# Kernel tuning notes

Measured on AMD Instinct MI355X. Metric: run time of the kernel, lower is better.

Reference implementation:

```python
import jax, jax.numpy as jnp
import numpy as np

TOP_K = 2
EPS = 1e-6

def setup_inputs() -> dict:
    key = jax.random.key(0)
    ks = jax.random.split(key, 6)
    Bt, S, D, E, R = 4, 4096, 1024, 8, 4
    s = lambda d: 1.0 / np.sqrt(d)
    return {
        "x": jax.random.normal(ks[0], (Bt, S, D), jnp.float32),
        "W_base": jax.random.normal(ks[1], (D, D), jnp.float32) * s(D),
        "b_base": jax.random.normal(ks[2], (D,), jnp.float32) * 0.02,
        "W_router": jax.random.normal(ks[3], (E, D), jnp.float32) * s(D),
        "A": jax.random.normal(ks[4], (E, D, R), jnp.float32) * s(D),
        "B": jax.random.normal(ks[5], (E, R, D), jnp.float32) * s(R),
    }

def reference(x, W_base, b_base, W_router, A, B):
    # frozen base linear: [b,s,d] @ [out,d]^T + bias
    base_out = jnp.einsum('bsd,od->bso', x, W_base) + b_base
    # router softmax gate over experts
    logits = jnp.einsum('bsd,ed->bse', x, W_router)
    gate = jax.nn.softmax(logits, axis=-1)
    # top-k scatter-mask (values kept are the gate values themselves)
    topv, topi = jax.lax.top_k(gate, TOP_K)                    # [b,s,k]
    mask = jnp.sum(jax.nn.one_hot(topi, gate.shape[-1], dtype=gate.dtype), axis=-2)
    gate = gate * mask
    gate = gate / (jnp.sum(gate, axis=-1, keepdims=True) + EPS)
    # batched rank-4 LoRA experts, gating applied in low-rank space
    h = jnp.einsum('bsd,edr->bser', x, A)                      # [b,s,E,r]
    hg = h * gate[..., None]                                   # weight before up-proj
    lora_out = jnp.einsum('bser,ero->bso', hg, B)
    return base_out + lora_out
```

## Files before the change

### kernel.cpp

```cpp
#include <hip/hip_runtime.h>
#include <cstdint>

typedef __attribute__((ext_vector_type(8))) short short8;
typedef __attribute__((ext_vector_type(4))) float f32x4;

__device__ inline unsigned short f2bf(float f){
  union { float f; uint32_t u; } v; v.f = f;
  uint32_t r = v.u + 0x7FFFu + ((v.u >> 16) & 1u);
  return (unsigned short)(r >> 16);
}

#define GLL(gp, lp) __builtin_amdgcn_global_load_lds(              \
    (const __attribute__((address_space(1))) void*)(gp),           \
    (__attribute__((address_space(3))) void*)(lp), 16, 0, 0)

__global__ __launch_bounds__(256) void kconv(const float* __restrict__ W,
                                             const float* __restrict__ A,
                                             const float* __restrict__ Bm,
                                             unsigned short* __restrict__ Wb,
                                             unsigned short* __restrict__ BTt,
                                             unsigned short* __restrict__ W2b){
  int i = blockIdx.x * 256 + threadIdx.x;
  Wb[i] = f2bf(W[i]);
  if (i < 32768){
    int o = i >> 5, c = i & 31;
    BTt[i] = f2bf(Bm[(size_t)c*1024 + o]);
    int n = i >> 10, d = i & 1023;
    W2b[i] = f2bf(A[(((size_t)(n>>2))*1024 + d)*4 + (n&3)]);
  }
}

__global__ __launch_bounds__(256) void kxl(const float* __restrict__ x,
                                           const float* __restrict__ Wr,
                                           unsigned short* __restrict__ xb,
                                           float* __restrict__ gate){
  __shared__ float wr[8192];
  const int tid  = threadIdx.x;
  const int lane = tid & 63;
  const int w    = tid >> 6;
  {
    const float4* s  = (const float4*)Wr;
    float4*       d4 = (float4*)wr;
    #pragma unroll
    for (int j=0;j<8;j++) d4[j*256+tid] = s[j*256+tid];
  }
  __syncthreads();
  const float4* wr4 = (const float4*)wr;
  #pragma unroll 1
  for (int tt=0; tt<4; tt++){
    const size_t tok = (size_t)blockIdx.x*16 + w*4 + tt;
    const float4* xr = (const float4*)(x + tok*1024);
    ushort4*      xd = (ushort4*)(xb + tok*1024);
    float4 xv[4];
    #pragma unroll
    for (int c=0;c<4;c++){
      xv[c] = xr[c*64 + lane];
      ushort4 o4; o4.x=f2bf(xv[c].x); o4.y=f2bf(xv[c].y);
      o4.z=f2bf(xv[c].z); o4.w=f2bf(xv[c].w);
      xd[c*64 + lane] = o4;
    }
    float p[8];
    #pragma unroll
    for (int e=0;e<8;e++){
      float a = 0.f;
      #pragma unroll
      for (int c=0;c<4;c++){
        float4 wv = wr4[e*256 + c*64 + lane];
        a += xv[c].x*wv.x + xv[c].y*wv.y + xv[c].z*wv.z + xv[c].w*wv.w;
      }
      p[e] = a;
    }
    #pragma unroll
    for (int off=32; off; off>>=1){
      #pragma unroll
      for (int e=0;e<8;e++) p[e] += __shfl_xor(p[e], off, 64);
    }
    if (lane == 0){
      float mx = p[0];
      #pragma unroll
      for (int e=1;e<8;e++) mx = fmaxf(mx, p[e]);
      float ex[8], s2 = 0.f;
      #pragma unroll
      for (int e=0;e<8;e++){ ex[e] = __expf(p[e]-mx); s2 += ex[e]; }
      int i1 = 0; float v1 = ex[0];
      #pragma unroll
      for (int e=1;e<8;e++) if (ex[e] > v1){ v1 = ex[e]; i1 = e; }
      int i2 = -1; float v2 = -1.f;
      #pragma unroll
      for (int e=0;e<8;e++) if (e != i1 && ex[e] > v2){ v2 = ex[e]; i2 = e; }
      float g1 = v1/s2, g2 = v2/s2;
      float rs = 1.f/(g1 + g2 + 1e-6f);
      float* go = gate + tok*8;
      #pragma unroll
      for (int e=0;e<8;e++) go[e] = (e==i1 ? g1 : (e==i2 ? g2 : 0.f)) * rs;
    }
  }
}

__global__ __launch_bounds__(256) void kh(const unsigned short* __restrict__ xbp,
                                          const unsigned short* __restrict__ W2b,
                                          const float* __restrict__ gate,
                                          unsigned short* __restrict__ HG){
  const int tid  = threadIdx.x;
  const int lane = tid & 63;
  const int wid  = tid >> 6;
  const int lrow = lane & 15;
  const int lk   = (lane >> 4) * 8;
  const int tok0 = blockIdx.x*64 + wid*16;
  f32x4 acc0 = {0.f,0.f,0.f,0.f}, acc1 = {0.f,0.f,0.f,0.f};
  const unsigned short* b0 = W2b + (size_t)lrow*1024 + lk;
  const unsigned short* b1 = W2b + (size_t)(16+lrow)*1024 + lk;
  const unsigned short* ar = xbp + (size_t)(tok0+lrow)*1024 + lk;
  #pragma unroll 4
  for (int ks=0; ks<32; ks++){
    short8 av  = *(const short8*)(ar + ks*32);
    short8 bv0 = *(const short8*)(b0 + ks*32);
    short8 bv1 = *(const short8*)(b1 + ks*32);
    acc0 = __builtin_amdgcn_mfma_f32_16x16x32_bf16(av, bv0, acc0, 0, 0, 0);
    acc1 = __builtin_amdgcn_mfma_f32_16x16x32_bf16(av, bv1, acc1, 0, 0, 0);
  }
  #pragma unroll
  for (int j=0;j<4;j++){
    int tok = tok0 + (lane>>4)*4 + j;
    float g0 = gate[(size_t)tok*8 + (lrow>>2)];
    float g1 = gate[(size_t)tok*8 + 4 + (lrow>>2)];
    HG[(size_t)tok*32 + lrow]      = f2bf(acc0[j]*g0);
    HG[(size_t)tok*32 + 16 + lrow] = f2bf(acc1[j]*g1);
  }
}

__global__ __launch_bounds__(512, 2) void kgemm2(const unsigned short* __restrict__ xb,
                                                 const unsigned short* __restrict__ Wb,
                                                 const unsigned short* __restrict__ BTt,
                                                 const unsigned short* __restrict__ HG,
                                                 const float* __restrict__ bias,
                                                 float* __restrict__ out){
  __shared__ char lds[65536];
  const int tid  = threadIdx.x;
  const int lane = tid & 63;
  const int w    = tid >> 6;
  const int xcd  = blockIdx.x & 7, jj = blockIdx.x >> 3;
  const int nblk = xcd >> 1;
  const int mblk = (xcd & 1) * 32 + jj;
  const int m0 = mblk << 8, n0 = nblk << 8;
  const int wm = w >> 2, wn = w & 3;
  const int lrow = lane & 15;
  const int lkb  = (lane >> 4) << 4;

  int offA[8], offB[4];
  #pragma unroll
  for (int fm=0; fm<8; fm++){ int r = wm*128 + fm*16 + lrow; offA[fm] = r*64 + (lkb ^ (((r>>1)&3)<<4)); }
  #pragma unroll
  for (int fn=0; fn<4; fn++){ int r = wn*64  + fn*16 + lrow; offB[fn] = r*64 + (lkb ^ (((r>>1)&3)<<4)); }

  const int Rb0 = (w&3)*16 + (w>>2)*128 + (lane>>2);
  const int Rb1 = Rb0 + 64;
  const int ob  = (lane&3)*16;
  const int sw0 = ((Rb0>>1)&3)<<4, sw1 = ((Rb1>>1)&3)<<4;
  const char* Ag0 = (const char*)xb + (size_t)(m0+Rb0)*2048 + (ob ^ sw0);
  const char* Ag1 = (const char*)xb + (size_t)(m0+Rb1)*2048 + (ob ^ sw1);
  const char* Bg0 = (const char*)Wb + (size_t)(n0+Rb0)*2048 + (ob ^ sw0);
  const char* Bg1 = (const char*)Wb + (size_t)(n0+Rb1)*2048 + (ob ^ sw1);
  const int dH0 = ((w&3)*16 + (w>>2)*128)*64 + lane*16;
  const int dH1 = dH0 + 4096;

  f32x4 acc[8][4];
  #pragma unroll
  for (int a=0;a<8;a++)
    #pragma unroll
    for (int b=0;b<4;b++) acc[a][b] = (f32x4){0.f,0.f,0.f,0.f};

  GLL(Ag0 +  0, lds + dH0);            GLL(Ag1 +  0, lds + dH1);
  GLL(Bg0 +  0, lds + 32768 + dH0);    GLL(Bg1 +  0, lds + 32768 + dH1);
  GLL(Ag0 + 64, lds + 16384 + dH0);    GLL(Bg0 + 64, lds + 49152 + dH0);

  #pragma unroll 1
  for (int t = 0; t < 32; ++t){
    const int s = t & 1;
    const char* Ab = lds + s*16384;
    const char* Bb = lds + 32768 + s*16384;
    if (t < 31){
      const int s1 = (t+1)&1;
      GLL(Ag1 + (t+1)*64, lds + s1*16384 + dH1);
      GLL(Bg1 + (t+1)*64, lds + 32768 + s1*16384 + dH1);
      asm volatile("s_waitcnt vmcnt(4)" ::: "memory");
    } else {
      asm volatile("s_waitcnt vmcnt(0)" ::: "memory");
    }
    __builtin_amdgcn_s_barrier();
    short8 bf[4];
    #pragma unroll
    for (int fn=0;fn<4;fn++) bf[fn] = *(const short8*)(Bb + offB[fn]);
    short8 af[4];
    #pragma unroll
    for (int fm=0;fm<4;fm++) af[fm] = *(const short8*)(Ab + offA[fm]);
    __builtin_amdgcn_s_setprio(1);
    #pragma unroll
    for (int fm=0;fm<4;fm++)
      #pragma unroll
      for (int fn=0;fn<4;fn++)
        acc[fm][fn] = __builtin_amdgcn_mfma_f32_16x16x32_bf16(af[fm], bf[fn], acc[fm][fn], 0, 0, 0);
    __builtin_amdgcn_s_setprio(0);
    __builtin_amdgcn_s_barrier();
    if (t < 30){
      const int s2 = t & 1;
      GLL(Ag0 + (t+2)*64, lds + s2*16384 + dH0);
      GLL(Bg0 + (t+2)*64, lds + 32768 + s2*16384 + dH0);
    }
    short8 ag[4];
    #pragma unroll
    for (int fm=0;fm<4;fm++) ag[fm] = *(const short8*)(Ab + offA[4+fm]);
    __builtin_amdgcn_s_setprio(1);
    #pragma unroll
    for (int fm=0;fm<4;fm++)
      #pragma unroll
      for (int fn=0;fn<4;fn++)
        acc[4+fm][fn] = __builtin_amdgcn_mfma_f32_16x16x32_bf16(ag[fm], bf[fn], acc[4+fm][fn], 0, 0, 0);
    __builtin_amdgcn_s_setprio(0);
    __builtin_amdgcn_s_barrier();
  }

  {
    const char* Hg0 = (const char*)HG  + (size_t)(m0+Rb0)*64 + (ob ^ sw0);
    const char* Hg1 = (const char*)HG  + (size_t)(m0+Rb1)*64 + (ob ^ sw1);
    const char* Tg0 = (const char*)BTt + (size_t)(n0+Rb0)*64 + (ob ^ sw0);
    const char* Tg1 = (const char*)BTt + (size_t)(n0+Rb1)*64 + (ob ^ sw1);
    GLL(Hg0, lds + dH0);          GLL(Hg1, lds + dH1);
    GLL(Tg0, lds + 32768 + dH0);  GLL(Tg1, lds + 32768 + dH1);
    asm volatile("s_waitcnt vmcnt(0)" ::: "memory");
    __builtin_amdgcn_s_barrier();
    short8 hb[4];
    #pragma unroll
    for (int fn=0;fn<4;fn++) hb[fn] = *(const short8*)(lds + 32768 + offB[fn]);
    #pragma unroll
    for (int fm=0;fm<8;fm++){
      short8 ha = *(const short8*)(lds + offA[fm]);
      #pragma unroll
      for (int fn=0;fn<4;fn++)
        acc[fm][fn] = __builtin_amdgcn_mfma_f32_16x16x32_bf16(ha, hb[fn], acc[fm][fn], 0, 0, 0);
    }
  }

  #pragma unroll
  for (int fn=0;fn<4;fn++){
    int col = n0 + wn*64 + fn*16 + lrow;
    float bv = bias[col];
    #pragma unroll
    for (int fm=0;fm<8;fm++){
      int rb = m0 + wm*128 + fm*16 + (lane>>4)*4;
      #pragma unroll
      for (int j=0;j<4;j++)
        out[(size_t)(rb+j)*1024 + col] = acc[fm][fn][j] + bv;
    }
  }
}

extern "C" void kernel_launch(void* const* d_in, const int* in_sizes, int n_in,
                              void* d_out, int out_size, void* d_ws, size_t ws_size,
                              hipStream_t stream){
  const float* x  = (const float*)d_in[0];
  const float* W  = (const float*)d_in[1];
  const float* bb = (const float*)d_in[2];
  const float* Wr = (const float*)d_in[3];
  const float* A  = (const float*)d_in[4];
  const float* Bm = (const float*)d_in[5];
  float* out = (float*)d_out;
  char* ws = (char*)d_ws;

  unsigned short* Wb   = (unsigned short*)(ws + 0);
  unsigned short* BTt  = (unsigned short*)(ws + 2097152);
  unsigned short* W2b  = (unsigned short*)(ws + 2162688);
  float*          gate = (float*)         (ws + 2228224);
  unsigned short* HG   = (unsigned short*)(ws + 2752512);
  unsigned short* xb   = (unsigned short*)(ws + 3801088);

  kconv<<<4096, 256, 0, stream>>>(W, A, Bm, Wb, BTt, W2b);
  kxl<<<1024, 256, 0, stream>>>(x, Wr, xb, gate);
  kh<<<256, 256, 0, stream>>>(xb, W2b, gate, HG);
  kgemm2<<<256, 512, 0, stream>>>(xb, Wb, BTt, HG, bb, out);
}
```

Before: 97.46 us.

## Rework router kernel and switch main GEMM to smaller 128x128 tiles

The router/convert kernel now assigns 8 lanes per token and 32 tokens per block, halving the block count and shortening the shuffle reduction. The main GEMM drops from 256x256 tiles with 512 threads and a double-buffered, hand-pipelined load schedule to 128x128 tiles with 256 threads, a single-buffered 64-wide K stage, an XOR swizzle and plain __syncthreads. The low-rank LoRA term is now loaded straight from global memory rather than staged through LDS. This trades the overlap of loads with MFMA and the reuse of larger tiles for more blocks and higher occupancy (4 blocks per CU), and it fetches more total global traffic.

```diff
diff --git a/kernel.cpp b/kernel.cpp
--- a/kernel.cpp
+++ b/kernel.cpp
@@ -30,14 +30,14 @@
   }
 }
 
-__global__ __launch_bounds__(256) void kxl(const float* __restrict__ x,
-                                           const float* __restrict__ Wr,
-                                           unsigned short* __restrict__ xb,
-                                           float* __restrict__ gate){
+__global__ __launch_bounds__(256) void kxl2(const float* __restrict__ x,
+                                            const float* __restrict__ Wr,
+                                            unsigned short* __restrict__ xb,
+                                            float* __restrict__ gate){
   __shared__ float wr[8192];
   const int tid  = threadIdx.x;
   const int lane = tid & 63;
-  const int w    = tid >> 6;
+  const int wid  = tid >> 6;
   {
     const float4* s  = (const float4*)Wr;
     float4*       d4 = (float4*)wr;
@@ -45,55 +45,46 @@
     for (int j=0;j<8;j++) d4[j*256+tid] = s[j*256+tid];
   }
   __syncthreads();
-  const float4* wr4 = (const float4*)wr;
-  #pragma unroll 1
-  for (int tt=0; tt<4; tt++){
-    const size_t tok = (size_t)blockIdx.x*16 + w*4 + tt;
-    const float4* xr = (const float4*)(x + tok*1024);
-    ushort4*      xd = (ushort4*)(xb + tok*1024);
-    float4 xv[4];
-    #pragma unroll
-    for (int c=0;c<4;c++){
-      xv[c] = xr[c*64 + lane];
-      ushort4 o4; o4.x=f2bf(xv[c].x); o4.y=f2bf(xv[c].y);
-      o4.z=f2bf(xv[c].z); o4.w=f2bf(xv[c].w);
-      xd[c*64 + lane] = o4;
-    }
-    float p[8];
+  const int tk  = lane >> 3, ln8 = lane & 7;
+  const size_t tok = (size_t)blockIdx.x*32 + wid*8 + tk;
+  const float4* xr = (const float4*)(x + tok*1024);
+  ushort4*      xd = (ushort4*)(xb + tok*1024);
+  const float4* wv = (const float4*)wr;
+  float p[8] = {0.f,0.f,0.f,0.f,0.f,0.f,0.f,0.f};
+  #pragma unroll 4
+  for (int it=0; it<32; it++){
+    float4 v = xr[it*8 + ln8];
+    ushort4 o; o.x=f2bf(v.x); o.y=f2bf(v.y); o.z=f2bf(v.z); o.w=f2bf(v.w);
+    xd[it*8 + ln8] = o;
     #pragma unroll
     for (int e=0;e<8;e++){
-      float a = 0.f;
-      #pragma unroll
-      for (int c=0;c<4;c++){
-        float4 wv = wr4[e*256 + c*64 + lane];
-        a += xv[c].x*wv.x + xv[c].y*wv.y + xv[c].z*wv.z + xv[c].w*wv.w;
-      }
-      p[e] = a;
-    }
-    #pragma unroll
-    for (int off=32; off; off>>=1){
-      #pragma unroll
-      for (int e=0;e<8;e++) p[e] += __shfl_xor(p[e], off, 64);
-    }
-    if (lane == 0){
-      float mx = p[0];
-      #pragma unroll
-      for (int e=1;e<8;e++) mx = fmaxf(mx, p[e]);
-      float ex[8], s2 = 0.f;
-      #pragma unroll
-      for (int e=0;e<8;e++){ ex[e] = __expf(p[e]-mx); s2 += ex[e]; }
-      int i1 = 0; float v1 = ex[0];
-      #pragma unroll
-      for (int e=1;e<8;e++) if (ex[e] > v1){ v1 = ex[e]; i1 = e; }
-      int i2 = -1; float v2 = -1.f;
-      #pragma unroll
-      for (int e=0;e<8;e++) if (e != i1 && ex[e] > v2){ v2 = ex[e]; i2 = e; }
-      float g1 = v1/s2, g2 = v2/s2;
-      float rs = 1.f/(g1 + g2 + 1e-6f);
-      float* go = gate + tok*8;
-      #pragma unroll
-      for (int e=0;e<8;e++) go[e] = (e==i1 ? g1 : (e==i2 ? g2 : 0.f)) * rs;
-    }
+      float4 wq = wv[e*256 + it*8 + ln8];
+      p[e] += v.x*wq.x + v.y*wq.y + v.z*wq.z + v.w*wq.w;
+    }
+  }
+  #pragma unroll
+  for (int off=1; off<8; off<<=1){
+    #pragma unroll
+    for (int e=0;e<8;e++) p[e] += __shfl_xor(p[e], off, 64);
+  }
+  if (ln8 == 0){
+    float mx = p[0];
+    #pragma unroll
+    for (int e=1;e<8;e++) mx = fmaxf(mx, p[e]);
+    float ex[8], s2 = 0.f;
+    #pragma unroll
+    for (int e=0;e<8;e++){ ex[e] = __expf(p[e]-mx); s2 += ex[e]; }
+    int i1 = 0; float v1 = ex[0];
+    #pragma unroll
+    for (int e=1;e<8;e++) if (ex[e] > v1){ v1 = ex[e]; i1 = e; }
+    int i2 = -1; float v2 = -1.f;
+    #pragma unroll
+    for (int e=0;e<8;e++) if (e != i1 && ex[e] > v2){ v2 = ex[e]; i2 = e; }
+    float g1 = v1/s2, g2 = v2/s2;
+    float rs = 1.f/(g1 + g2 + 1e-6f);
+    float* go = gate + tok*8;
+    #pragma unroll
+    for (int e=0;e<8;e++) go[e] = (e==i1 ? g1 : (e==i2 ? g2 : 0.f)) * rs;
   }
 }
 
@@ -129,116 +120,85 @@
   }
 }
 
-__global__ __launch_bounds__(512, 2) void kgemm2(const unsigned short* __restrict__ xb,
+__global__ __launch_bounds__(256, 4) void kgemm7(const unsigned short* __restrict__ xb,
                                                  const unsigned short* __restrict__ Wb,
                                                  const unsigned short* __restrict__ BTt,
                                                  const unsigned short* __restrict__ HG,
                                                  const float* __restrict__ bias,
                                                  float* __restrict__ out){
-  __shared__ char lds[65536];
+  __shared__ __attribute__((aligned(128))) char lds[32768];
   const int tid  = threadIdx.x;
   const int lane = tid & 63;
   const int w    = tid >> 6;
-  const int xcd  = blockIdx.x & 7, jj = blockIdx.x >> 3;
-  const int nblk = xcd >> 1;
-  const int mblk = (xcd & 1) * 32 + jj;
-  const int m0 = mblk << 8, n0 = nblk << 8;
-  const int wm = w >> 2, wn = w & 3;
+  const int mblk = blockIdx.x & 127;
+  const int nblk = blockIdx.x >> 7;
+  const int m0 = mblk << 7, n0 = nblk << 7;
+  const int wm = w >> 1, wn = w & 1;
   const int lrow = lane & 15;
-  const int lkb  = (lane >> 4) << 4;
-
-  int offA[8], offB[4];
-  #pragma unroll
-  for (int fm=0; fm<8; fm++){ int r = wm*128 + fm*16 + lrow; offA[fm] = r*64 + (lkb ^ (((r>>1)&3)<<4)); }
-  #pragma unroll
-  for (int fn=0; fn<4; fn++){ int r = wn*64  + fn*16 + lrow; offB[fn] = r*64 + (lkb ^ (((r>>1)&3)<<4)); }
-
-  const int Rb0 = (w&3)*16 + (w>>2)*128 + (lane>>2);
-  const int Rb1 = Rb0 + 64;
-  const int ob  = (lane&3)*16;
-  const int sw0 = ((Rb0>>1)&3)<<4, sw1 = ((Rb1>>1)&3)<<4;
-  const char* Ag0 = (const char*)xb + (size_t)(m0+Rb0)*2048 + (ob ^ sw0);
-  const char* Ag1 = (const char*)xb + (size_t)(m0+Rb1)*2048 + (ob ^ sw1);
-  const char* Bg0 = (const char*)Wb + (size_t)(n0+Rb0)*2048 + (ob ^ sw0);
-  const char* Bg1 = (const char*)Wb + (size_t)(n0+Rb1)*2048 + (ob ^ sw1);
-  const int dH0 = ((w&3)*16 + (w>>2)*128)*64 + lane*16;
-  const int dH1 = dH0 + 4096;
-
-  f32x4 acc[8][4];
-  #pragma unroll
-  for (int a=0;a<8;a++)
-    #pragma unroll
-    for (int b=0;b<4;b++) acc[a][b] = (f32x4){0.f,0.f,0.f,0.f};
-
-  GLL(Ag0 +  0, lds + dH0);            GLL(Ag1 +  0, lds + dH1);
-  GLL(Bg0 +  0, lds + 32768 + dH0);    GLL(Bg1 +  0, lds + 32768 + dH1);
-  GLL(Ag0 + 64, lds + 16384 + dH0);    GLL(Bg0 + 64, lds + 49152 + dH0);
+  const int q    = lane >> 4;
+
+  const int rowL = lane >> 3;
+  const int colb = ((lane & 7) ^ rowL) << 4;
+  const int rb   = w * 32;
+  const char* Ag = (const char*)xb + ((size_t)(m0 + rb + rowL) << 11) + colb;
+  const char* Bg = (const char*)Wb + ((size_t)(n0 + rb + rowL) << 11) + colb;
+  char* Ad = lds +         rb*128 + lane*16;
+  char* Bd = lds + 16384 + rb*128 + lane*16;
+
+  int offA[4][2], offB[4][2];
+  #pragma unroll
+  for (int f=0; f<4; f++){
+    int ra = wm*64 + f*16 + lrow;
+    int rbn = wn*64 + f*16 + lrow;
+    #pragma unroll
+    for (int kk=0; kk<2; kk++){
+      offA[f][kk] =         ra*128  + ((((kk*4+q) ^ (ra  & 7)) << 4));
+      offB[f][kk] = 16384 + rbn*128 + ((((kk*4+q) ^ (rbn & 7)) << 4));
+    }
+  }
+
+  f32x4 acc[4][4];
+  #pragma unroll
+  for (int a2=0;a2<4;a2++)
+    #pragma unroll
+    for (int b2=0;b2<4;b2++) acc[a2][b2] = (f32x4){0.f,0.f,0.f,0.f};
 
   #pragma unroll 1
-  for (int t = 0; t < 32; ++t){
-    const int s = t & 1;
-    const char* Ab = lds + s*16384;
-    const char* Bb = lds + 32768 + s*16384;
-    if (t < 31){
-      const int s1 = (t+1)&1;
-      GLL(Ag1 + (t+1)*64, lds + s1*16384 + dH1);
-      GLL(Bg1 + (t+1)*64, lds + 32768 + s1*16384 + dH1);
-      asm volatile("s_waitcnt vmcnt(4)" ::: "memory");
-    } else {
-      asm volatile("s_waitcnt vmcnt(0)" ::: "memory");
-    }
-    __builtin_amdgcn_s_barrier();
-    short8 bf[4];
-    #pragma unroll
-    for (int fn=0;fn<4;fn++) bf[fn] = *(const short8*)(Bb + offB[fn]);
-    short8 af[4];
-    #pragma unroll
-    for (int fm=0;fm<4;fm++) af[fm] = *(const short8*)(Ab + offA[fm]);
-    __builtin_amdgcn_s_setprio(1);
+  for (int t = 0; t < 16; ++t){
+    __syncthreads();
+    #pragma unroll
+    for (int i=0;i<4;i++) GLL(Ag + (size_t)i*16384 + t*128, Ad + i*1024);
+    #pragma unroll
+    for (int i=0;i<4;i++) GLL(Bg + (size_t)i*16384 + t*128, Bd + i*1024);
+    __syncthreads();
+    #pragma unroll
+    for (int kk=0; kk<2; kk++){
+      short8 a[4], b[4];
+      #pragma unroll
+      for (int f=0; f<4; f++){
+        a[f] = *(const short8*)(lds + offA[f][kk]);
+        b[f] = *(const short8*)(lds + offB[f][kk]);
+      }
+      #pragma unroll
+      for (int fm=0;fm<4;fm++)
+        #pragma unroll
+        for (int fn=0;fn<4;fn++)
+          acc[fm][fn] = __builtin_amdgcn_mfma_f32_16x16x32_bf16(a[fm], b[fn], acc[fm][fn], 0, 0, 0);
+    }
+  }
+
+  {
+    short8 ha[4], hb[4];
+    #pragma unroll
+    for (int f=0; f<4; f++){
+      ha[f] = *(const short8*)(HG  + (size_t)(m0 + wm*64 + f*16 + lrow)*32 + q*8);
+      hb[f] = *(const short8*)(BTt + (size_t)(n0 + wn*64 + f*16 + lrow)*32 + q*8);
+    }
     #pragma unroll
     for (int fm=0;fm<4;fm++)
       #pragma unroll
       for (int fn=0;fn<4;fn++)
-        acc[fm][fn] = __builtin_amdgcn_mfma_f32_16x16x32_bf16(af[fm], bf[fn], acc[fm][fn], 0, 0, 0);
-    __builtin_amdgcn_s_setprio(0);
-    __builtin_amdgcn_s_barrier();
-    if (t < 30){
-      const int s2 = t & 1;
-      GLL(Ag0 + (t+2)*64, lds + s2*16384 + dH0);
-      GLL(Bg0 + (t+2)*64, lds + 32768 + s2*16384 + dH0);
-    }
-    short8 ag[4];
-    #pragma unroll
-    for (int fm=0;fm<4;fm++) ag[fm] = *(const short8*)(Ab + offA[4+fm]);
-    __builtin_amdgcn_s_setprio(1);
-    #pragma unroll
-    for (int fm=0;fm<4;fm++)
-      #pragma unroll
-      for (int fn=0;fn<4;fn++)
-        acc[4+fm][fn] = __builtin_amdgcn_mfma_f32_16x16x32_bf16(ag[fm], bf[fn], acc[4+fm][fn], 0, 0, 0);
-    __builtin_amdgcn_s_setprio(0);
-    __builtin_amdgcn_s_barrier();
-  }
-
-  {
-    const char* Hg0 = (const char*)HG  + (size_t)(m0+Rb0)*64 + (ob ^ sw0);
-    const char* Hg1 = (const char*)HG  + (size_t)(m0+Rb1)*64 + (ob ^ sw1);
-    const char* Tg0 = (const char*)BTt + (size_t)(n0+Rb0)*64 + (ob ^ sw0);
-    const char* Tg1 = (const char*)BTt + (size_t)(n0+Rb1)*64 + (ob ^ sw1);
-    GLL(Hg0, lds + dH0);          GLL(Hg1, lds + dH1);
-    GLL(Tg0, lds + 32768 + dH0);  GLL(Tg1, lds + 32768 + dH1);
-    asm volatile("s_waitcnt vmcnt(0)" ::: "memory");
-    __builtin_amdgcn_s_barrier();
-    short8 hb[4];
-    #pragma unroll
-    for (int fn=0;fn<4;fn++) hb[fn] = *(const short8*)(lds + 32768 + offB[fn]);
-    #pragma unroll
-    for (int fm=0;fm<8;fm++){
-      short8 ha = *(const short8*)(lds + offA[fm]);
-      #pragma unroll
-      for (int fn=0;fn<4;fn++)
-        acc[fm][fn] = __builtin_amdgcn_mfma_f32_16x16x32_bf16(ha, hb[fn], acc[fm][fn], 0, 0, 0);
-    }
+        acc[fm][fn] = __builtin_amdgcn_mfma_f32_16x16x32_bf16(ha[fm], hb[fn], acc[fm][fn], 0, 0, 0);
   }
 
   #pragma unroll
@@ -246,11 +206,11 @@
     int col = n0 + wn*64 + fn*16 + lrow;
     float bv = bias[col];
     #pragma unroll
-    for (int fm=0;fm<8;fm++){
-      int rb = m0 + wm*128 + fm*16 + (lane>>4)*4;
+    for (int fm=0;fm<4;fm++){
+      int rbo = m0 + wm*64 + fm*16 + q*4;
       #pragma unroll
       for (int j=0;j<4;j++)
-        out[(size_t)(rb+j)*1024 + col] = acc[fm][fn][j] + bv;
+        out[(size_t)(rbo+j)*1024 + col] = acc[fm][fn][j] + bv;
     }
   }
 }
@@ -275,7 +235,7 @@
   unsigned short* xb   = (unsigned short*)(ws + 3801088);
 
   kconv<<<4096, 256, 0, stream>>>(W, A, Bm, Wb, BTt, W2b);
-  kxl<<<1024, 256, 0, stream>>>(x, Wr, xb, gate);
+  kxl2<<<512, 256, 0, stream>>>(x, Wr, xb, gate);
   kh<<<256, 256, 0, stream>>>(xb, W2b, gate, HG);
-  kgemm2<<<256, 512, 0, stream>>>(xb, Wb, BTt, HG, bb, out);
-}
+  kgemm7<<<1024, 256, 0, stream>>>(xb, Wb, BTt, HG, bb, out);
+}
```

Measured after the change: 92.54 us. 5.0% less time.
